# Performance work log

Hardware: AMD Instinct MI355X
Metric: run time of the kernel (lower is better)

## Reference

```python
import jax, jax.numpy as jnp
import numpy as np
import math

B, L, D = 8, 2048, 256


def setup_inputs() -> dict:
    key = jax.random.key(0)
    ks = jax.random.split(key, 8)
    return {
        "query": jax.random.normal(ks[0], (B, L, D), dtype=jnp.float32),
        "key": jax.random.normal(ks[1], (B, L, D), dtype=jnp.float32),
        "value": jax.random.normal(ks[2], (B, L, D), dtype=jnp.float32),
        "mask": jax.random.randint(ks[3], (B, L), 0, 2, dtype=jnp.int32),
        "Wq_w": jax.random.normal(ks[4], (D, D), dtype=jnp.float32) * 0.05,
        "Wq_b": jax.random.normal(ks[5], (D,), dtype=jnp.float32) * 0.05,
        "Wk_w": jax.random.normal(ks[6], (D, D), dtype=jnp.float32) * 0.05,
        "Wk_b": jax.random.normal(ks[7], (D,), dtype=jnp.float32) * 0.05,
    }


def reference(query, key, value, mask, Wq_w, Wq_b, Wk_w, Wk_b):
    d = query.shape[-1]
    q = query @ Wq_w.T + Wq_b            # [B, Lq, D]
    k = key @ Wk_w.T + Wk_b              # [B, Lk, D]
    scores = jnp.einsum("bqd,bkd->bqk", q, k) / math.sqrt(d)  # [B, Lq, Lk]
    m = mask.astype(scores.dtype)[:, None, :]                  # [B, 1, Lk]
    # multiplicative then additive masking, as in original
    scores = jnp.where(m == 0, jnp.asarray(-1e9, scores.dtype), scores * m)
    attn = jax.nn.softmax(scores, axis=-1)
    return jnp.einsum("bqk,bkd->bqd", attn, value)
```

## Files before the change

### kernel.cpp

```cpp
#include <hip/hip_runtime.h>
#include <stdint.h>
#include <stddef.h>

#define B_ 8
#define L_ 2048
#define D_ 256
#define KSPLIT 4
#define KRANGE 512
#define KTILE 32
#define NITER 16

#define WAITVM(n) __builtin_amdgcn_s_waitcnt(0x0F70 | (n))

typedef __bf16 bf16x8 __attribute__((ext_vector_type(8)));
typedef float floatx4 __attribute__((ext_vector_type(4)));
typedef float floatx16 __attribute__((ext_vector_type(16)));
typedef _Float16 half4_t __attribute__((ext_vector_type(4)));

__device__ __forceinline__ short f2bf(float f) {
    union { float f; uint32_t u; } v; v.f = f;
    return (short)((v.u + 0x8000u) >> 16);
}

__device__ __forceinline__ uint32_t pack2bf(float a, float b) {
    union { float f; uint32_t u; } x, y; x.f = a; y.f = b;
    return ((x.u + 0x8000u) >> 16) | ((y.u + 0x8000u) & 0xFFFF0000u);
}

__device__ __forceinline__ uint32_t cvtpk_bf16(float lo, float hi2) {
    uint32_t w;
    asm("v_cvt_pk_bf16_f32 %0, %1, %2" : "=v"(w) : "v"(lo), "v"(hi2));
    return w;
}

__device__ __forceinline__ void pl32swap(uint32_t &a, uint32_t &b) {
    asm("v_permlane32_swap_b32 %0, %1" : "+v"(a), "+v"(b));
}

__device__ __forceinline__ void async16(const void* g, void* l) {
    __builtin_amdgcn_global_load_lds(
        (__attribute__((address_space(1))) void*)g,
        (__attribute__((address_space(3))) void*)l,
        16, 0, 0);
}

__global__ __launch_bounds__(256, 3) void proj_kernel(
    const float* __restrict__ Xq, const float* __restrict__ Xk,
    const float* __restrict__ Wq, const float* __restrict__ Wk,
    const float* __restrict__ bq, const float* __restrict__ bk,
    short* __restrict__ Oq, short* __restrict__ Ok)
{
    const float* X    = blockIdx.y ? Xk : Xq;
    const float* W    = blockIdx.y ? Wk : Wq;
    const float* bias = blockIdx.y ? bk : bq;
    short* Out        = blockIdx.y ? Ok : Oq;

    __shared__ uint32_t As[2][64 * 20];
    __shared__ uint32_t Ws[2][256 * 20];

    const int tid  = threadIdx.x;
    const int wid  = tid >> 6;
    const int lane = tid & 63;
    const int m16  = lane & 15;
    const int quad = lane >> 4;
    const int row0 = blockIdx.x * 64;
    const int ar = tid >> 2, cg = tid & 3;

    floatx4 acc[16];
    const floatx4 z4 = {0.f, 0.f, 0.f, 0.f};
#pragma unroll
    for (int i = 0; i < 16; i++) acc[i] = z4;

    {
        const float* srcA = X + (size_t)(row0 + ar) * D_ + cg * 8;
        float4 a = *(const float4*)srcA, b2 = *(const float4*)(srcA + 4);
        uint4 u; u.x = pack2bf(a.x, a.y); u.y = pack2bf(a.z, a.w);
        u.z = pack2bf(b2.x, b2.y); u.w = pack2bf(b2.z, b2.w);
        *(uint4*)&As[0][ar * 20 + cg * 4] = u;
#pragma unroll
        for (int p = 0; p < 4; p++) {
            const float* srcW = W + (size_t)(p * 64 + ar) * D_ + cg * 8;
            float4 wa = *(const float4*)srcW, wb = *(const float4*)(srcW + 4);
            uint4 w; w.x = pack2bf(wa.x, wa.y); w.y = pack2bf(wa.z, wa.w);
            w.z = pack2bf(wb.x, wb.y); w.w = pack2bf(wb.z, wb.w);
            *(uint4*)&Ws[0][(p * 64 + ar) * 20 + cg * 4] = w;
        }
    }
    __syncthreads();

    for (int kc = 0; kc < 8; kc++) {
        const int buf = kc & 1;
        float4 na, nb, nwa[4], nwb[4];
        if (kc < 7) {
            const int k1 = (kc + 1) * 32;
            const float* srcA = X + (size_t)(row0 + ar) * D_ + k1 + cg * 8;
            na = *(const float4*)srcA; nb = *(const float4*)(srcA + 4);
#pragma unroll
            for (int p = 0; p < 4; p++) {
                const float* srcW = W + (size_t)(p * 64 + ar) * D_ + k1 + cg * 8;
                nwa[p] = *(const float4*)srcW; nwb[p] = *(const float4*)(srcW + 4);
            }
        }
        bf16x8 af = *(const bf16x8*)&As[buf][(wid * 16 + m16) * 20 + quad * 4];
#pragma unroll
        for (int n = 0; n < 16; n++) {
            bf16x8 bfr = *(const bf16x8*)&Ws[buf][(n * 16 + m16) * 20 + quad * 4];
            acc[n] = __builtin_amdgcn_mfma_f32_16x16x32_bf16(af, bfr, acc[n], 0, 0, 0);
        }
        if (kc < 7) {
            uint4 u; u.x = pack2bf(na.x, na.y); u.y = pack2bf(na.z, na.w);
            u.z = pack2bf(nb.x, nb.y); u.w = pack2bf(nb.z, nb.w);
            *(uint4*)&As[buf ^ 1][ar * 20 + cg * 4] = u;
#pragma unroll
            for (int p = 0; p < 4; p++) {
                uint4 w; w.x = pack2bf(nwa[p].x, nwa[p].y); w.y = pack2bf(nwa[p].z, nwa[p].w);
                w.z = pack2bf(nwb[p].x, nwb[p].y); w.w = pack2bf(nwb[p].z, nwb[p].w);
                *(uint4*)&Ws[buf ^ 1][(p * 64 + ar) * 20 + cg * 4] = w;
            }
        }
        __syncthreads();
    }
#pragma unroll
    for (int n = 0; n < 16; n++) {
        const int col = n * 16 + m16;
        const float bv = bias[col];
#pragma unroll
        for (int r = 0; r < 4; r++) {
            const int row = row0 + wid * 16 + quad * 4 + r;
            Out[(size_t)row * D_ + col] = f2bf(acc[n][r] + bv);
        }
    }
}

__global__ __launch_bounds__(256, 2) void vtrans_kernel(
    const float* __restrict__ V, short* __restrict__ Vt)
{
    __shared__ uint32_t T[256 * 20];
    const int tid = threadIdx.x;
    const int b  = blockIdx.y;
    const int l0 = blockIdx.x * 32;
    const int r2 = tid >> 4;
    const int dg = tid & 15;
    const int lp = r2 ^ ((dg & 3) << 2);
#pragma unroll
    for (int p = 0; p < 4; p++) {
        int d0 = (dg + p * 16) * 4;
        const float* src = V + ((size_t)b * L_ + l0 + r2 * 2) * D_ + d0;
        float4 e0 = *(const float4*)src;
        float4 e1 = *(const float4*)(src + D_);
        T[(d0 + 0) * 20 + lp] = pack2bf(e0.x, e1.x);
        T[(d0 + 1) * 20 + lp] = pack2bf(e0.y, e1.y);
        T[(d0 + 2) * 20 + lp] = pack2bf(e0.z, e1.z);
        T[(d0 + 3) * 20 + lp] = pack2bf(e0.w, e1.w);
    }
    __syncthreads();
#pragma unroll
    for (int p = 0; p < 4; p++) {
        int d = (tid >> 2) + p * 64;
        int c = tid & 3;
        int cp = c ^ ((d >> 2) & 3);
        uint4 u = *(const uint4*)&T[d * 20 + cp * 4];
        *(uint4*)(Vt + ((size_t)b * D_ + d) * L_ + l0 + c * 8) = u;
    }
}

__global__ __launch_bounds__(256, 2) void flash_kernel(
    const short* __restrict__ Qb, const short* __restrict__ Kb,
    const short* __restrict__ Vt, const int* __restrict__ mask,
    float* __restrict__ Out, _Float16* __restrict__ Part,
    float* __restrict__ Lpart)
{
    __shared__ short Ks[2][KTILE * 256];
    __shared__ short Vs[2][256 * KTILE];

    const int tid  = threadIdx.x;
    const int wid  = tid >> 6;
    const int lane = tid & 63;
    const int l31  = lane & 31;
    const int hi   = lane >> 5;
    const int b  = blockIdx.x;
    const int q0 = blockIdx.y * 128;
    const int z  = blockIdx.z;

    const short* kbase = Kb + ((size_t)b * L_ + z * KRANGE) * D_;
    const short* vbase = Vt + (size_t)b * D_ * L_;
    const int*   mg    = mask + b * L_ + z * KRANGE;

    bf16x8 qf[16];
    {
        const short* qrow = Qb + ((size_t)b * L_ + q0 + wid * 32 + l31) * D_ + hi * 8;
#pragma unroll
        for (int dt = 0; dt < 16; dt++)
            qf[dt] = *(const bf16x8*)(qrow + dt * 16);
    }

    uint32_t mbits = 0;
#pragma unroll
    for (int t = 0; t < NITER; t++)
        mbits |= (mg[t * KTILE + l31] != 0 ? 1u : 0u) << t;

    floatx16 o[8];
#pragma unroll
    for (int n = 0; n < 8; n++)
#pragma unroll
        for (int r = 0; r < 16; r++) o[n][r] = 0.f;
    float rsum = 0.f;

    auto stageK = [&](int t, int bufi) {
        short* kl = &Ks[bufi][0];
#pragma unroll
        for (int c = 0; c < 4; c++) {
            int unit = wid * 4 + c;
            int row = unit * 2 + hi;
            int g = l31 ^ (row & 7) ^ ((row >> 3) & 3);
            async16(kbase + (size_t)(t * KTILE + row) * D_ + g * 8, kl + unit * 512);
        }
    };
    auto stageV = [&](int t, int bufi) {
        short* vl = &Vs[bufi][0];
#pragma unroll
        for (int c = 0; c < 4; c++) {
            int unit = wid * 4 + c;
            int d = unit * 16 + (lane >> 2);
            int g = (lane & 3) ^ ((lane >> 3) & 3) ^ ((lane >> 5) & 1);
            async16(vbase + (size_t)d * L_ + z * KRANGE + t * KTILE + g * 8, vl + unit * 512);
        }
    };

    stageK(0, 0);
    stageV(0, 0);
    WAITVM(4);
    __builtin_amdgcn_s_barrier();

    const float C2 = 0.09016844f;
    bf16x8 pfA, pfB;

    for (int t = 0; t < NITER; t++) {
        const int buf = t & 1;
        if (t + 1 < NITER) stageK(t + 1, buf ^ 1);
        const short* kl = &Ks[buf][0];

        floatx16 s0, s1;
#pragma unroll
        for (int r = 0; r < 16; r++) { s0[r] = 0.f; s1[r] = 0.f; }
        __builtin_amdgcn_s_setprio(1);
#pragma unroll
        for (int dt = 0; dt < 16; dt += 2) {
            int g0 = (dt * 2 + hi) ^ (l31 & 7) ^ ((l31 >> 3) & 3);
            int g1 = ((dt + 1) * 2 + hi) ^ (l31 & 7) ^ ((l31 >> 3) & 3);
            bf16x8 kf0 = *(const bf16x8*)(kl + l31 * 256 + g0 * 8);
            bf16x8 kf1 = *(const bf16x8*)(kl + l31 * 256 + g1 * 8);
            s0 = __builtin_amdgcn_mfma_f32_32x32x16_bf16(kf0, qf[dt], s0, 0, 0, 0);
            s1 = __builtin_amdgcn_mfma_f32_32x32x16_bf16(kf1, qf[dt + 1], s1, 0, 0, 0);
        }
        __builtin_amdgcn_s_setprio(0);

        if (t > 0) {
            const short* vl = &Vs[buf ^ 1][0];
            __builtin_amdgcn_s_setprio(1);
#pragma unroll
            for (int n = 0; n < 8; n++) {
                int d = n * 32 + l31;
#pragma unroll
                for (int kh = 0; kh < 2; kh++) {
                    int g2 = (kh * 2 + hi) ^ ((l31 >> 1) & 3) ^ ((l31 >> 3) & 1);
                    bf16x8 vf = *(const bf16x8*)(vl + d * 32 + g2 * 8);
                    o[n] = __builtin_amdgcn_mfma_f32_32x32x16_bf16(kh ? pfB : pfA, vf, o[n], 0, 0, 0);
                }
            }
            __builtin_amdgcn_s_setprio(0);
        }

        if (t + 1 < NITER) {
            __builtin_amdgcn_s_barrier();
            stageV(t + 1, buf ^ 1);
        }

        uint32_t mb = (uint32_t)__ballot((mbits >> t) & 1) >> (hi * 4);
        uint32_t w[8];
#pragma unroll
        for (int i = 0; i < 8; i++) {
            const int r0 = 2 * i, r1 = 2 * i + 1;
            const int k0 = (r0 & 3) + 8 * (r0 >> 2);
            float sv0 = s0[r0] + s1[r0];
            float sv1 = s0[r1] + s1[r1];
            float e0 = ((mb >> k0) & 1) ? exp2f(sv0 * C2) : 0.f;
            float e1 = ((mb >> (k0 + 1)) & 1) ? exp2f(sv1 * C2) : 0.f;
            rsum += e0 + e1;
            w[i] = cvtpk_bf16(e0, e1);
        }
        pl32swap(w[0], w[2]); pl32swap(w[1], w[3]);
        pl32swap(w[4], w[6]); pl32swap(w[5], w[7]);
        {
            union { uint32_t u[4]; bf16x8 v; } ua, ub;
            ua.u[0] = w[0]; ua.u[1] = w[1]; ua.u[2] = w[2]; ua.u[3] = w[3];
            ub.u[0] = w[4]; ub.u[1] = w[5]; ub.u[2] = w[6]; ub.u[3] = w[7];
            pfA = ua.v; pfB = ub.v;
        }

        if (t + 1 < NITER) WAITVM(4); else WAITVM(0);
        __builtin_amdgcn_s_barrier();
    }

    {
        const short* vl = &Vs[(NITER - 1) & 1][0];
        __builtin_amdgcn_s_setprio(1);
#pragma unroll
        for (int n = 0; n < 8; n++) {
            int d = n * 32 + l31;
#pragma unroll
            for (int kh = 0; kh < 2; kh++) {
                int g2 = (kh * 2 + hi) ^ ((l31 >> 1) & 3) ^ ((l31 >> 3) & 1);
                bf16x8 vf = *(const bf16x8*)(vl + d * 32 + g2 * 8);
                o[n] = __builtin_amdgcn_mfma_f32_32x32x16_bf16(kh ? pfB : pfA, vf, o[n], 0, 0, 0);
            }
        }
        __builtin_amdgcn_s_setprio(0);
    }

    rsum += __shfl_xor(rsum, 32);

    const size_t BLD = (size_t)B_ * L_ * D_;
    const size_t rowbase = (size_t)b * L_ + q0 + wid * 32;
    if (z == 0) {
        float* po = Out + rowbase * D_;
#pragma unroll
        for (int n = 0; n < 8; n++)
#pragma unroll
            for (int r = 0; r < 16; r++) {
                int q = (r & 3) + 8 * (r >> 2) + 4 * hi;
                po[(size_t)q * D_ + n * 32 + l31] = o[n][r];
            }
    } else {
        _Float16* pp = Part + (size_t)(z - 1) * BLD + rowbase * D_;
#pragma unroll
        for (int n = 0; n < 8; n++)
#pragma unroll
            for (int r = 0; r < 16; r++) {
                int q = (r & 3) + 8 * (r >> 2) + 4 * hi;
                pp[(size_t)q * D_ + n * 32 + l31] = (_Float16)o[n][r];
            }
    }
    if (lane < 32) {
        Lpart[(size_t)z * (B_ * L_) + rowbase + lane] = rsum;
    }
}

__global__ __launch_bounds__(256) void norm_kernel(
    float* __restrict__ Out, const _Float16* __restrict__ Part,
    const float* __restrict__ Lpart)
{
    const int idx = blockIdx.x * 256 + threadIdx.x;
    const int row = idx >> 6;
    const int c   = (idx & 63) * 4;
    const size_t off = (size_t)row * D_ + c;
    const size_t BLD = (size_t)B_ * L_ * D_;
    float4 acc = *(float4*)(Out + off);
#pragma unroll
    for (int zz = 0; zz < 3; zz++) {
        half4_t h = *(const half4_t*)(Part + zz * BLD + off);
        acc.x += (float)h.x; acc.y += (float)h.y;
        acc.z += (float)h.z; acc.w += (float)h.w;
    }
    const int BL = B_ * L_;
    float l = Lpart[row] + Lpart[BL + row] + Lpart[2 * BL + row] + Lpart[3 * BL + row];
    float inv = 1.0f / l;
    acc.x *= inv; acc.y *= inv; acc.z *= inv; acc.w *= inv;
    *(float4*)(Out + off) = acc;
}

extern "C" void kernel_launch(void* const* d_in, const int* in_sizes, int n_in,
                              void* d_out, int out_size, void* d_ws, size_t ws_size,
                              hipStream_t stream) {
    const float* query = (const float*)d_in[0];
    const float* key   = (const float*)d_in[1];
    const float* value = (const float*)d_in[2];
    const int*   mask  = (const int*)d_in[3];
    const float* Wq_w  = (const float*)d_in[4];
    const float* Wq_b  = (const float*)d_in[5];
    const float* Wk_w  = (const float*)d_in[6];
    const float* Wk_b  = (const float*)d_in[7];
    float* out = (float*)d_out;

    const size_t BLD = (size_t)B_ * L_ * D_;
    short* qb = (short*)d_ws;
    short* kb = qb + BLD;
    short* vt = kb + BLD;
    _Float16* part = (_Float16*)(vt + BLD);
    float* lpart = (float*)(part + 3 * BLD);

    proj_kernel<<<dim3(256, 2), 256, 0, stream>>>(query, key, Wq_w, Wk_w, Wq_b, Wk_b, qb, kb);
    vtrans_kernel<<<dim3(64, 8), 256, 0, stream>>>(value, vt);
    flash_kernel<<<dim3(8, 16, 4), 256, 0, stream>>>(qb, kb, vt, mask, out, part, lpart);
    norm_kernel<<<dim3((B_ * L_ * D_ / 4) / 256), 256, 0, stream>>>(out, part, lpart);
}
```

Baseline: 189.9 us.

## Fuse projection and V-transpose launches; re-pipeline flash K/V prefetch with one barrier per tile

The projection and V-transpose kernels become one launch, with even and odd blocks doing the two jobs, so one kernel launch and its tail are gone. The flash loop is unrolled by two, with precomputed byte offsets and XOR-swizzled LDS addresses. The K and V loads for the next tile are issued together at the top of each iteration, and one __syncthreads replaces the split barrier and explicit waitcnt scheme. In exchange, the first iteration does a PV multiply with a zeroed P, and the last iteration prefetches a K tile past its range. Correctness also depends on __syncthreads waiting for the async LDS loads to finish.

```diff
diff --git a/kernel.cpp b/kernel.cpp
--- a/kernel.cpp
+++ b/kernel.cpp
@@ -10,8 +10,6 @@
 #define KTILE 32
 #define NITER 16
 
-#define WAITVM(n) __builtin_amdgcn_s_waitcnt(0x0F70 | (n))
-
 typedef __bf16 bf16x8 __attribute__((ext_vector_type(8)));
 typedef float floatx4 __attribute__((ext_vector_type(4)));
 typedef float floatx16 __attribute__((ext_vector_type(16)));
@@ -44,26 +42,65 @@
         16, 0, 0);
 }
 
-__global__ __launch_bounds__(256, 3) void proj_kernel(
+__global__ __launch_bounds__(256, 3) void prep_kernel(
     const float* __restrict__ Xq, const float* __restrict__ Xk,
     const float* __restrict__ Wq, const float* __restrict__ Wk,
     const float* __restrict__ bq, const float* __restrict__ bk,
-    short* __restrict__ Oq, short* __restrict__ Ok)
+    const float* __restrict__ V,
+    short* __restrict__ Oq, short* __restrict__ Ok, short* __restrict__ Vt)
 {
-    const float* X    = blockIdx.y ? Xk : Xq;
-    const float* W    = blockIdx.y ? Wk : Wq;
-    const float* bias = blockIdx.y ? bk : bq;
-    short* Out        = blockIdx.y ? Ok : Oq;
-
-    __shared__ uint32_t As[2][64 * 20];
-    __shared__ uint32_t Ws[2][256 * 20];
-
-    const int tid  = threadIdx.x;
+    __shared__ uint32_t shm[2 * 64 * 20 + 2 * 256 * 20];
+    const int bid = blockIdx.x;
+    const int tid = threadIdx.x;
+
+    if (bid & 1) {
+        uint32_t* T = shm;
+        const int vb = bid >> 1;
+        const int b  = vb >> 6;
+        const int l0 = (vb & 63) * 32;
+        const int r2 = tid >> 4;
+        const int dg = tid & 15;
+        const int lp = r2 ^ ((dg & 3) << 2);
+#pragma unroll
+        for (int p = 0; p < 4; p++) {
+            int d0 = (dg + p * 16) * 4;
+            const float* src = V + ((size_t)b * L_ + l0 + r2 * 2) * D_ + d0;
+            float4 e0 = *(const float4*)src;
+            float4 e1 = *(const float4*)(src + D_);
+            T[(d0 + 0) * 20 + lp] = pack2bf(e0.x, e1.x);
+            T[(d0 + 1) * 20 + lp] = pack2bf(e0.y, e1.y);
+            T[(d0 + 2) * 20 + lp] = pack2bf(e0.z, e1.z);
+            T[(d0 + 3) * 20 + lp] = pack2bf(e0.w, e1.w);
+        }
+        __syncthreads();
+#pragma unroll
+        for (int p = 0; p < 4; p++) {
+            int d = (tid >> 2) + p * 64;
+            int c = tid & 3;
+            int cp = c ^ ((d >> 2) & 3);
+            uint4 u = *(const uint4*)&T[d * 20 + cp * 4];
+            *(uint4*)(Vt + ((size_t)b * D_ + d) * L_ + l0 + c * 8) = u;
+        }
+        return;
+    }
+
+    const int pb = bid >> 1;
+    const int py = pb >> 8;
+    const int px = pb & 255;
+
+    const float* X    = py ? Xk : Xq;
+    const float* W    = py ? Wk : Wq;
+    const float* bias = py ? bk : bq;
+    short* Out        = py ? Ok : Oq;
+
+    uint32_t* As = shm;
+    uint32_t* Ws = shm + 2 * 64 * 20;
+
     const int wid  = tid >> 6;
     const int lane = tid & 63;
     const int m16  = lane & 15;
     const int quad = lane >> 4;
-    const int row0 = blockIdx.x * 64;
+    const int row0 = px * 64;
     const int ar = tid >> 2, cg = tid & 3;
 
     floatx4 acc[16];
@@ -76,14 +113,14 @@
         float4 a = *(const float4*)srcA, b2 = *(const float4*)(srcA + 4);
         uint4 u; u.x = pack2bf(a.x, a.y); u.y = pack2bf(a.z, a.w);
         u.z = pack2bf(b2.x, b2.y); u.w = pack2bf(b2.z, b2.w);
-        *(uint4*)&As[0][ar * 20 + cg * 4] = u;
+        *(uint4*)&As[ar * 20 + cg * 4] = u;
 #pragma unroll
         for (int p = 0; p < 4; p++) {
             const float* srcW = W + (size_t)(p * 64 + ar) * D_ + cg * 8;
             float4 wa = *(const float4*)srcW, wb = *(const float4*)(srcW + 4);
             uint4 w; w.x = pack2bf(wa.x, wa.y); w.y = pack2bf(wa.z, wa.w);
             w.z = pack2bf(wb.x, wb.y); w.w = pack2bf(wb.z, wb.w);
-            *(uint4*)&Ws[0][(p * 64 + ar) * 20 + cg * 4] = w;
+            *(uint4*)&Ws[(p * 64 + ar) * 20 + cg * 4] = w;
         }
     }
     __syncthreads();
@@ -101,21 +138,21 @@
                 nwa[p] = *(const float4*)srcW; nwb[p] = *(const float4*)(srcW + 4);
             }
         }
-        bf16x8 af = *(const bf16x8*)&As[buf][(wid * 16 + m16) * 20 + quad * 4];
+        bf16x8 af = *(const bf16x8*)&As[buf * 1280 + (wid * 16 + m16) * 20 + quad * 4];
 #pragma unroll
         for (int n = 0; n < 16; n++) {
-            bf16x8 bfr = *(const bf16x8*)&Ws[buf][(n * 16 + m16) * 20 + quad * 4];
+            bf16x8 bfr = *(const bf16x8*)&Ws[buf * 5120 + (n * 16 + m16) * 20 + quad * 4];
             acc[n] = __builtin_amdgcn_mfma_f32_16x16x32_bf16(af, bfr, acc[n], 0, 0, 0);
         }
         if (kc < 7) {
             uint4 u; u.x = pack2bf(na.x, na.y); u.y = pack2bf(na.z, na.w);
             u.z = pack2bf(nb.x, nb.y); u.w = pack2bf(nb.z, nb.w);
-            *(uint4*)&As[buf ^ 1][ar * 20 + cg * 4] = u;
+            *(uint4*)&As[(buf ^ 1) * 1280 + ar * 20 + cg * 4] = u;
 #pragma unroll
             for (int p = 0; p < 4; p++) {
                 uint4 w; w.x = pack2bf(nwa[p].x, nwa[p].y); w.y = pack2bf(nwa[p].z, nwa[p].w);
                 w.z = pack2bf(nwb[p].x, nwb[p].y); w.w = pack2bf(nwb[p].z, nwb[p].w);
-                *(uint4*)&Ws[buf ^ 1][(p * 64 + ar) * 20 + cg * 4] = w;
+                *(uint4*)&Ws[(buf ^ 1) * 5120 + (p * 64 + ar) * 20 + cg * 4] = w;
             }
         }
         __syncthreads();
@@ -129,38 +166,6 @@
             const int row = row0 + wid * 16 + quad * 4 + r;
             Out[(size_t)row * D_ + col] = f2bf(acc[n][r] + bv);
         }
-    }
-}
-
-__global__ __launch_bounds__(256, 2) void vtrans_kernel(
-    const float* __restrict__ V, short* __restrict__ Vt)
-{
-    __shared__ uint32_t T[256 * 20];
-    const int tid = threadIdx.x;
-    const int b  = blockIdx.y;
-    const int l0 = blockIdx.x * 32;
-    const int r2 = tid >> 4;
-    const int dg = tid & 15;
-    const int lp = r2 ^ ((dg & 3) << 2);
-#pragma unroll
-    for (int p = 0; p < 4; p++) {
-        int d0 = (dg + p * 16) * 4;
-        const float* src = V + ((size_t)b * L_ + l0 + r2 * 2) * D_ + d0;
-        float4 e0 = *(const float4*)src;
-        float4 e1 = *(const float4*)(src + D_);
-        T[(d0 + 0) * 20 + lp] = pack2bf(e0.x, e1.x);
-        T[(d0 + 1) * 20 + lp] = pack2bf(e0.y, e1.y);
-        T[(d0 + 2) * 20 + lp] = pack2bf(e0.z, e1.z);
-        T[(d0 + 3) * 20 + lp] = pack2bf(e0.w, e1.w);
-    }
-    __syncthreads();
-#pragma unroll
-    for (int p = 0; p < 4; p++) {
-        int d = (tid >> 2) + p * 64;
-        int c = tid & 3;
-        int cp = c ^ ((d >> 2) & 3);
-        uint4 u = *(const uint4*)&T[d * 20 + cp * 4];
-        *(uint4*)(Vt + ((size_t)b * D_ + d) * L_ + l0 + c * 8) = u;
     }
 }
 
@@ -182,9 +187,9 @@
     const int q0 = blockIdx.y * 128;
     const int z  = blockIdx.z;
 
-    const short* kbase = Kb + ((size_t)b * L_ + z * KRANGE) * D_;
-    const short* vbase = Vt + (size_t)b * D_ * L_;
-    const int*   mg    = mask + b * L_ + z * KRANGE;
+    const char* kgb = (const char*)(Kb + ((size_t)b * L_ + z * KRANGE) * D_);
+    const char* vgb = (const char*)(Vt + (size_t)b * D_ * L_ + z * KRANGE);
+    const int*  mg  = mask + b * L_ + z * KRANGE;
 
     bf16x8 qf[16];
     {
@@ -206,114 +211,112 @@
         for (int r = 0; r < 16; r++) o[n][r] = 0.f;
     float rsum = 0.f;
 
-    auto stageK = [&](int t, int bufi) {
-        short* kl = &Ks[bufi][0];
-#pragma unroll
-        for (int c = 0; c < 4; c++) {
-            int unit = wid * 4 + c;
-            int row = unit * 2 + hi;
-            int g = l31 ^ (row & 7) ^ ((row >> 3) & 3);
-            async16(kbase + (size_t)(t * KTILE + row) * D_ + g * 8, kl + unit * 512);
-        }
-    };
-    auto stageV = [&](int t, int bufi) {
-        short* vl = &Vs[bufi][0];
-#pragma unroll
-        for (int c = 0; c < 4; c++) {
-            int unit = wid * 4 + c;
-            int d = unit * 16 + (lane >> 2);
-            int g = (lane & 3) ^ ((lane >> 3) & 3) ^ ((lane >> 5) & 1);
-            async16(vbase + (size_t)d * L_ + z * KRANGE + t * KTILE + g * 8, vl + unit * 512);
-        }
-    };
-
-    stageK(0, 0);
-    stageV(0, 0);
-    WAITVM(4);
-    __builtin_amdgcn_s_barrier();
+    const int KBb = l31 * 512 + ((((l31 & 7) ^ ((l31 >> 3) & 3)) ^ hi) << 4);
+    const int VBb = l31 * 64 + (((((l31 >> 1) & 3) ^ ((l31 >> 3) & 1)) ^ hi) << 4);
+
+    int koff[4], voff[4];
+#pragma unroll
+    for (int c = 0; c < 4; c++) {
+        int row = wid * 8 + c * 2 + hi;
+        int gk = l31 ^ (row & 7) ^ ((row >> 3) & 3);
+        koff[c] = row * 512 + gk * 16;
+        int d = (wid * 4 + c) * 16 + (lane >> 2);
+        int gv = (lane & 3) ^ ((lane >> 3) & 3) ^ ((lane >> 5) & 1);
+        voff[c] = d * (L_ * 2) + gv * 16;
+    }
+
+#pragma unroll
+    for (int c = 0; c < 4; c++)
+        async16(kgb + koff[c], &Ks[0][0] + (wid * 4 + c) * 512);
+#pragma unroll
+    for (int c = 0; c < 4; c++)
+        async16(vgb + voff[c], &Vs[1][0] + (wid * 4 + c) * 512);
+    __builtin_amdgcn_s_waitcnt(0x0F70);
+    __syncthreads();
 
     const float C2 = 0.09016844f;
     bf16x8 pfA, pfB;
-
-    for (int t = 0; t < NITER; t++) {
-        const int buf = t & 1;
-        if (t + 1 < NITER) stageK(t + 1, buf ^ 1);
-        const short* kl = &Ks[buf][0];
-
-        floatx16 s0, s1;
-#pragma unroll
-        for (int r = 0; r < 16; r++) { s0[r] = 0.f; s1[r] = 0.f; }
+    {
+        union { uint32_t u[4]; bf16x8 v; } zz;
+        zz.u[0] = 0; zz.u[1] = 0; zz.u[2] = 0; zz.u[3] = 0;
+        pfA = zz.v; pfB = zz.v;
+    }
+
+    for (int t2 = 0; t2 < NITER; t2 += 2) {
+#pragma unroll
+        for (int half = 0; half < 2; half++) {
+            const int t = t2 + half;
+            const int buf = half;
+
+            {
+                const char* kp = kgb + (size_t)(t + 1) * (KTILE * D_ * 2);
+                const char* vp = vgb + (size_t)t * (KTILE * 2);
+#pragma unroll
+                for (int c = 0; c < 4; c++)
+                    async16(kp + koff[c], &Ks[buf ^ 1][0] + (wid * 4 + c) * 512);
+#pragma unroll
+                for (int c = 0; c < 4; c++)
+                    async16(vp + voff[c], &Vs[buf][0] + (wid * 4 + c) * 512);
+            }
+
+            const char* kl = (const char*)&Ks[buf][0];
+            floatx16 s0, s1;
+#pragma unroll
+            for (int r = 0; r < 16; r++) { s0[r] = 0.f; s1[r] = 0.f; }
+            __builtin_amdgcn_s_setprio(1);
+#pragma unroll
+            for (int dt = 0; dt < 16; dt += 2) {
+                bf16x8 kf0 = *(const bf16x8*)(kl + (KBb ^ (dt << 5)));
+                bf16x8 kf1 = *(const bf16x8*)(kl + (KBb ^ ((dt + 1) << 5)));
+                s0 = __builtin_amdgcn_mfma_f32_32x32x16_bf16(kf0, qf[dt], s0, 0, 0, 0);
+                s1 = __builtin_amdgcn_mfma_f32_32x32x16_bf16(kf1, qf[dt + 1], s1, 0, 0, 0);
+            }
+
+            const char* vl = (const char*)&Vs[buf ^ 1][0];
+#pragma unroll
+            for (int n = 0; n < 8; n++) {
+                bf16x8 vf0 = *(const bf16x8*)(vl + (VBb ^ (n << 11)));
+                bf16x8 vf1 = *(const bf16x8*)(vl + (VBb ^ ((n << 11) | 32)));
+                o[n] = __builtin_amdgcn_mfma_f32_32x32x16_bf16(pfA, vf0, o[n], 0, 0, 0);
+                o[n] = __builtin_amdgcn_mfma_f32_32x32x16_bf16(pfB, vf1, o[n], 0, 0, 0);
+            }
+            __builtin_amdgcn_s_setprio(0);
+
+            uint32_t mb = (uint32_t)__ballot((mbits >> t) & 1) >> (hi * 4);
+            uint32_t w[8];
+#pragma unroll
+            for (int i = 0; i < 8; i++) {
+                const int r0 = 2 * i, r1 = 2 * i + 1;
+                const int k0 = (r0 & 3) + 8 * (r0 >> 2);
+                float sv0 = s0[r0] + s1[r0];
+                float sv1 = s0[r1] + s1[r1];
+                float e0 = ((mb >> k0) & 1) ? exp2f(sv0 * C2) : 0.f;
+                float e1 = ((mb >> (k0 + 1)) & 1) ? exp2f(sv1 * C2) : 0.f;
+                rsum += e0 + e1;
+                w[i] = cvtpk_bf16(e0, e1);
+            }
+            pl32swap(w[0], w[2]); pl32swap(w[1], w[3]);
+            pl32swap(w[4], w[6]); pl32swap(w[5], w[7]);
+            {
+                union { uint32_t u[4]; bf16x8 v; } ua, ub;
+                ua.u[0] = w[0]; ua.u[1] = w[1]; ua.u[2] = w[2]; ua.u[3] = w[3];
+                ub.u[0] = w[4]; ub.u[1] = w[5]; ub.u[2] = w[6]; ub.u[3] = w[7];
+                pfA = ua.v; pfB = ub.v;
+            }
+
+            __syncthreads();
+        }
+    }
+
+    {
+        const char* vl = (const char*)&Vs[1][0];
         __builtin_amdgcn_s_setprio(1);
 #pragma unroll
-        for (int dt = 0; dt < 16; dt += 2) {
-            int g0 = (dt * 2 + hi) ^ (l31 & 7) ^ ((l31 >> 3) & 3);
-            int g1 = ((dt + 1) * 2 + hi) ^ (l31 & 7) ^ ((l31 >> 3) & 3);
-            bf16x8 kf0 = *(const bf16x8*)(kl + l31 * 256 + g0 * 8);
-            bf16x8 kf1 = *(const bf16x8*)(kl + l31 * 256 + g1 * 8);
-            s0 = __builtin_amdgcn_mfma_f32_32x32x16_bf16(kf0, qf[dt], s0, 0, 0, 0);
-            s1 = __builtin_amdgcn_mfma_f32_32x32x16_bf16(kf1, qf[dt + 1], s1, 0, 0, 0);
-        }
-        __builtin_amdgcn_s_setprio(0);
-
-        if (t > 0) {
-            const short* vl = &Vs[buf ^ 1][0];
-            __builtin_amdgcn_s_setprio(1);
-#pragma unroll
-            for (int n = 0; n < 8; n++) {
-                int d = n * 32 + l31;
-#pragma unroll
-                for (int kh = 0; kh < 2; kh++) {
-                    int g2 = (kh * 2 + hi) ^ ((l31 >> 1) & 3) ^ ((l31 >> 3) & 1);
-                    bf16x8 vf = *(const bf16x8*)(vl + d * 32 + g2 * 8);
-                    o[n] = __builtin_amdgcn_mfma_f32_32x32x16_bf16(kh ? pfB : pfA, vf, o[n], 0, 0, 0);
-                }
-            }
-            __builtin_amdgcn_s_setprio(0);
-        }
-
-        if (t + 1 < NITER) {
-            __builtin_amdgcn_s_barrier();
-            stageV(t + 1, buf ^ 1);
-        }
-
-        uint32_t mb = (uint32_t)__ballot((mbits >> t) & 1) >> (hi * 4);
-        uint32_t w[8];
-#pragma unroll
-        for (int i = 0; i < 8; i++) {
-            const int r0 = 2 * i, r1 = 2 * i + 1;
-            const int k0 = (r0 & 3) + 8 * (r0 >> 2);
-            float sv0 = s0[r0] + s1[r0];
-            float sv1 = s0[r1] + s1[r1];
-            float e0 = ((mb >> k0) & 1) ? exp2f(sv0 * C2) : 0.f;
-            float e1 = ((mb >> (k0 + 1)) & 1) ? exp2f(sv1 * C2) : 0.f;
-            rsum += e0 + e1;
-            w[i] = cvtpk_bf16(e0, e1);
-        }
-        pl32swap(w[0], w[2]); pl32swap(w[1], w[3]);
-        pl32swap(w[4], w[6]); pl32swap(w[5], w[7]);
-        {
-            union { uint32_t u[4]; bf16x8 v; } ua, ub;
-            ua.u[0] = w[0]; ua.u[1] = w[1]; ua.u[2] = w[2]; ua.u[3] = w[3];
-            ub.u[0] = w[4]; ub.u[1] = w[5]; ub.u[2] = w[6]; ub.u[3] = w[7];
-            pfA = ua.v; pfB = ub.v;
-        }
-
-        if (t + 1 < NITER) WAITVM(4); else WAITVM(0);
-        __builtin_amdgcn_s_barrier();
-    }
-
-    {
-        const short* vl = &Vs[(NITER - 1) & 1][0];
-        __builtin_amdgcn_s_setprio(1);
-#pragma unroll
         for (int n = 0; n < 8; n++) {
-            int d = n * 32 + l31;
-#pragma unroll
-            for (int kh = 0; kh < 2; kh++) {
-                int g2 = (kh * 2 + hi) ^ ((l31 >> 1) & 3) ^ ((l31 >> 3) & 1);
-                bf16x8 vf = *(const bf16x8*)(vl + d * 32 + g2 * 8);
-                o[n] = __builtin_amdgcn_mfma_f32_32x32x16_bf16(kh ? pfB : pfA, vf, o[n], 0, 0, 0);
-            }
+            bf16x8 vf0 = *(const bf16x8*)(vl + (VBb ^ (n << 11)));
+            bf16x8 vf1 = *(const bf16x8*)(vl + (VBb ^ ((n << 11) | 32)));
+            o[n] = __builtin_amdgcn_mfma_f32_32x32x16_bf16(pfA, vf0, o[n], 0, 0, 0);
+            o[n] = __builtin_amdgcn_mfma_f32_32x32x16_bf16(pfB, vf1, o[n], 0, 0, 0);
         }
         __builtin_amdgcn_s_setprio(0);
     }
@@ -389,8 +392,8 @@
     _Float16* part = (_Float16*)(vt + BLD);
     float* lpart = (float*)(part + 3 * BLD);
 
-    proj_kernel<<<dim3(256, 2), 256, 0, stream>>>(query, key, Wq_w, Wk_w, Wq_b, Wk_b, qb, kb);
-    vtrans_kernel<<<dim3(64, 8), 256, 0, stream>>>(value, vt);
+    prep_kernel<<<dim3(1024), 256, 0, stream>>>(query, key, Wq_w, Wk_w, Wq_b, Wk_b,
+                                                value, qb, kb, vt);
     flash_kernel<<<dim3(8, 16, 4), 256, 0, stream>>>(qb, kb, vt, mask, out, part, lpart);
     norm_kernel<<<dim3((B_ * L_ * D_ / 4) / 256), 256, 0, stream>>>(out, part, lpart);
 }
```

After: 199.4 us. +5.0%, slower.
